# Performance work log

Hardware: AMD Instinct MI355X
Metric: run time of the kernel (lower is better)

## Reference

```python
import jax, jax.numpy as jnp
import numpy as np

N_HEAD = 16
MASK_VALUE = -10000.0


def setup_inputs() -> dict:
    key = jax.random.key(0)
    k1, k2, k3 = jax.random.split(key, 3)
    B, S, D = 2, 2048, 1024
    x = jax.random.normal(k1, (B, S, D), dtype=jnp.float32)
    W_qkv = jax.random.normal(k2, (D, 3 * D), dtype=jnp.float32) * 0.02
    b_qkv = jnp.zeros((3 * D,), dtype=jnp.float32)
    W_out = jax.random.normal(k3, (D, D), dtype=jnp.float32) * 0.02
    b_out = jnp.zeros((D,), dtype=jnp.float32)
    return {"x": x, "W_qkv": W_qkv, "b_qkv": b_qkv, "W_out": W_out, "b_out": b_out}


def reference(x, W_qkv, b_qkv, W_out, b_out):
    B, S, D = x.shape
    H = N_HEAD
    hd = D // H
    # fused QKV projection
    qkv = x @ W_qkv + b_qkv                      # [B, S, 3D]
    q, k, v = jnp.split(qkv, 3, axis=-1)
    # split heads -> [B, H, S, hd]
    def split_heads(t):
        return t.reshape(B, S, H, hd).transpose(0, 2, 1, 3)
    q, k, v = split_heads(q), split_heads(k), split_heads(v)
    # scaled causal attention with explicit mask-fill (matches ops.attention)
    scale = 1.0 / jnp.sqrt(jnp.asarray(hd, dtype=x.dtype))
    w = jnp.einsum('bhqd,bhkd->bhqk', q, k) * scale   # [B, H, S, S]
    causal = jnp.tril(jnp.ones((S, S), dtype=bool))    # [S, S]
    w = jnp.where(causal, w, jnp.asarray(MASK_VALUE, dtype=w.dtype))
    a = jax.nn.softmax(w, axis=-1)
    o = jnp.einsum('bhqk,bhkd->bhqd', a, v)            # [B, H, S, hd]
    # merge heads -> [B, S, D]
    o = o.transpose(0, 2, 1, 3).reshape(B, S, D)
    out = o @ W_out + b_out
    return out
```

## Files before the change

kernel.cpp:

```cpp
#include <hip/hip_runtime.h>
#include <hip/hip_bf16.h>
#include <stdint.h>

#define BATCH 2
#define SEQ   2048
#define DIM   1024
#define NH    16
#define HD    64
#define MVAL  (-10000.0f)

#if __has_builtin(__builtin_amdgcn_exp2f)
#define EXP2(x) __builtin_amdgcn_exp2f(x)
#define QSCALE  (0.125f * 1.44269504f)
#else
#define EXP2(x) __expf(x)
#define QSCALE  0.125f
#endif

typedef __attribute__((ext_vector_type(8))) short bf16x8;
typedef __attribute__((ext_vector_type(4))) float f32x4;
typedef unsigned short u16;

static __device__ __forceinline__ u16 f2bf(float f) {
  union { float f; uint32_t u; } c; c.f = f;
  uint32_t x = c.u;
  return (u16)((x + 0x7fffu + ((x >> 16) & 1u)) >> 16);
}

static __device__ __forceinline__ uint32_t pk2(float a, float b) {
  __hip_bfloat162 h = __float22bfloat162_rn(make_float2(a, b));
  union { __hip_bfloat162 h; uint32_t u; } c; c.h = h;
  return c.u;
}

static __device__ __forceinline__ int swz128(int row, int chunk) {
  return row * 128 + (((chunk ^ (row & 7)) & 7) << 4);
}

static __device__ __forceinline__ void gload_lds16(const void* g, void* l) {
  __builtin_amdgcn_global_load_lds((const __attribute__((address_space(1))) void*)g,
                                   (__attribute__((address_space(3))) void*)l, 16, 0, 0);
}

__global__ void cvt_kernel(const float* __restrict__ in, u16* __restrict__ out, int n4) {
  int i = blockIdx.x * blockDim.x + threadIdx.x;
  if (i < n4) {
    float4 v = reinterpret_cast<const float4*>(in)[i];
    reinterpret_cast<uint2*>(out)[i] = make_uint2(pk2(v.x, v.y), pk2(v.z, v.w));
  }
}

__global__ void transpose_cvt_kernel(const float* __restrict__ in, u16* __restrict__ out,
                                     int R, int C) {
  __shared__ float tile[32][33];
  int c0 = blockIdx.x * 32, r0 = blockIdx.y * 32;
  int tx = threadIdx.x, ty = threadIdx.y;
#pragma unroll
  for (int i = 0; i < 32; i += 8)
    tile[ty + i][tx] = in[(size_t)(r0 + ty + i) * C + c0 + tx];
  __syncthreads();
#pragma unroll
  for (int i = 0; i < 32; i += 8)
    out[(size_t)(c0 + ty + i) * R + r0 + tx] = f2bf(tile[tx][ty + i]);
}

__global__ void vtrans_kernel(const u16* __restrict__ Vi, u16* __restrict__ Vo) {
  __shared__ __align__(16) char t[8192];
  int tid = threadIdx.x;
  int bh = blockIdx.y, s0 = blockIdx.x * 64;
  const u16* src = Vi + ((size_t)bh * SEQ + s0) * HD;
#pragma unroll
  for (int i = 0; i < 2; i++) {
    int r = i * 32 + (tid >> 3), ch = tid & 7;
    uint4 v = *reinterpret_cast<const uint4*>(src + (size_t)r * HD + ch * 8);
    *reinterpret_cast<uint4*>(t + swz128(r, ch)) = v;
  }
  __syncthreads();
  int d = tid >> 2, sc = tid & 3;
  u16 vals[16];
#pragma unroll
  for (int j = 0; j < 16; j++) {
    int s = sc * 16 + j;
    vals[j] = *reinterpret_cast<const u16*>(
        t + s * 128 + ((((d >> 3) ^ (s & 7)) & 7) << 4) + (d & 7) * 2);
  }
  u16* dst = Vo + ((size_t)bh * HD + d) * SEQ + s0 + sc * 16;
  *reinterpret_cast<uint4*>(dst) = *reinterpret_cast<const uint4*>(vals);
  *reinterpret_cast<uint4*>(dst + 8) = *reinterpret_cast<const uint4*>(vals + 8);
}

template <int EPI>
__global__ __launch_bounds__(256, 2) void gemm_bt_kernel(
    const u16* __restrict__ A, const u16* __restrict__ Bt,
    const float* __restrict__ bias, float* __restrict__ Cout,
    u16* __restrict__ Qo, u16* __restrict__ Ko, u16* __restrict__ Vo,
    int M, int N, int K) {
  __shared__ __align__(16) char lds[32768];
  char* As = lds;
  char* Bs = lds + 16384;
  int tid = threadIdx.x;
  int lane = tid & 63, l15 = lane & 15, l4 = lane >> 4;
  int w = tid >> 6, wr = w >> 1, wc = w & 1;
  int m0 = blockIdx.y * 128, n0 = blockIdx.x * 128;
  int srow = tid >> 3, sch = tid & 7;
  int sc_swz = ((sch ^ (srow & 7)) << 3);

  const u16* Ap = A + (size_t)(m0 + srow) * K + sc_swz;
  const u16* Bp = Bt + (size_t)(n0 + srow) * K + sc_swz;

  f32x4 acc[4][4] = {};

  for (int k0 = 0; k0 < K; k0 += 64) {
    __syncthreads();
#pragma unroll
    for (int i = 0; i < 4; i++) {
      gload_lds16(Ap + (size_t)i * 32 * K + k0, As + i * 4096 + tid * 16);
      gload_lds16(Bp + (size_t)i * 32 * K + k0, Bs + i * 4096 + tid * 16);
    }
    __syncthreads();
#pragma unroll
    for (int ks = 0; ks < 2; ks++) {
      int ch = ks * 4 + l4;
      bf16x8 af[4], bfv[4];
#pragma unroll
      for (int mi = 0; mi < 4; mi++)
        af[mi] = *reinterpret_cast<const bf16x8*>(As + swz128(wr * 64 + mi * 16 + l15, ch));
#pragma unroll
      for (int nj = 0; nj < 4; nj++)
        bfv[nj] = *reinterpret_cast<const bf16x8*>(Bs + swz128(wc * 64 + nj * 16 + l15, ch));
#pragma unroll
      for (int nj = 0; nj < 4; nj++)
#pragma unroll
        for (int mi = 0; mi < 4; mi++)
          acc[nj][mi] = __builtin_amdgcn_mfma_f32_16x16x32_bf16(bfv[nj], af[mi], acc[nj][mi], 0, 0, 0);
    }
  }

#pragma unroll
  for (int nj = 0; nj < 4; nj++) {
    int nb = n0 + wc * 64 + nj * 16 + l4 * 4;
    float4 bv = *reinterpret_cast<const float4*>(bias + nb);
#pragma unroll
    for (int mi = 0; mi < 4; mi++) {
      int m = m0 + wr * 64 + mi * 16 + l15;
      f32x4 a = acc[nj][mi];
      float v0 = a[0] + bv.x, v1 = a[1] + bv.y, v2 = a[2] + bv.z, v3 = a[3] + bv.w;
      if (EPI == 1) {
        *reinterpret_cast<float4*>(Cout + (size_t)m * N + nb) = make_float4(v0, v1, v2, v3);
      } else {
        int b = m >> 11, s = m & 2047;
        int sec = nb >> 10, c = nb & 1023, h = c >> 6, d = c & 63;
        size_t bh = (size_t)(b * NH + h);
        u16* dst;
        float scl;
        if (sec == 0)      { dst = Qo; scl = QSCALE; }
        else if (sec == 1) { dst = Ko; scl = 1.0f; }
        else               { dst = Vo; scl = 1.0f; }
        *reinterpret_cast<uint2*>(dst + (bh * SEQ + s) * HD + d) =
            make_uint2(pk2(v0 * scl, v1 * scl), pk2(v2 * scl, v3 * scl));
      }
    }
  }
}

__global__ __launch_bounds__(256, 2) void attn_kernel(
    const u16* __restrict__ Q, const u16* __restrict__ K,
    const u16* __restrict__ Vt, u16* __restrict__ O) {
  __shared__ __align__(16) char lds[81920];
  int tid = threadIdx.x, lane = tid & 63, w = tid >> 6;
  int l15 = lane & 15, l4 = lane >> 4;
  int sub = w & 1, par = w >> 1;
  int blk = blockIdx.x;
  int bh = (blk & 7) * 4 + ((blk >> 3) & 3);
  int p = blk >> 5;
  const u16* Qh = Q + (size_t)bh * SEQ * HD;
  const u16* Kh = K + (size_t)bh * SEQ * HD;
  const u16* Vh = Vt + (size_t)bh * HD * SEQ;
  char* Pw = lds + 65536 + w * 4096;
  int srow = tid >> 3, sch = tid & 7;
  int b_ = bh >> 4, h_ = bh & 15;

  bf16x8 onesf;
#pragma unroll
  for (int j = 0; j < 8; j++) onesf[j] = (short)0x3F80;

  auto stageKV = [&](int b, int T) {
    const u16* Kt = Kh + (size_t)T * 128 * HD;
    const u16* Vs = Vh + (size_t)T * 128;
    char* Kb = lds + b * 16384;
    char* Vb = lds + 32768 + b * 16384;
#pragma unroll
    for (int i = 0; i < 4; i++) {
      int row = i * 32 + srow;
      int c = (sch ^ (row & 7)) << 3;
      gload_lds16(Kt + (size_t)row * HD + c, Kb + row * 128 + sch * 16);
    }
#pragma unroll
    for (int sv = 0; sv < 2; sv++)
#pragma unroll
      for (int i = 0; i < 2; i++) {
        int d = i * 32 + srow;
        int c = (sch ^ (d & 7)) << 3;
        gload_lds16(Vs + (size_t)d * SEQ + sv * 64 + c, Vb + sv * 8192 + d * 128 + sch * 16);
      }
  };

  int buf = 0;
  stageKV(0, 0);
  __syncthreads();

  for (int pass = 0; pass < 2; pass++) {
    int qt = (pass == 0) ? (31 - p) : p;
    int nT = (qt + 2) >> 1;
    int qb = qt * 64 + sub * 32;

    bf16x8 qf[2][2];
#pragma unroll
    for (int mi = 0; mi < 2; mi++)
#pragma unroll
      for (int ks = 0; ks < 2; ks++)
        qf[mi][ks] = *reinterpret_cast<const bf16x8*>(
            Qh + (size_t)(qb + mi * 16 + l15) * HD + ks * 32 + l4 * 8);

    float mrun[2] = {-1e30f, -1e30f};
    f32x4 oacc[4][2] = {};
    f32x4 acc_l[2] = {};

    for (int T = 0; T < nT; T++) {
      int nxt = (T + 1 < nT) ? (T + 1) : (pass == 0 ? 0 : -1);
      if (nxt >= 0) stageKV(buf ^ 1, nxt);

      char* Kw = lds + buf * 16384 + par * 8192;
      char* Vw = lds + 32768 + buf * 16384 + par * 8192;
      int kvb = T * 128 + par * 64;

      f32x4 s[4][2] = {};
      __builtin_amdgcn_s_setprio(1);
#pragma unroll
      for (int ks = 0; ks < 2; ks++)
#pragma unroll
        for (int nj = 0; nj < 4; nj++) {
          bf16x8 kf = *reinterpret_cast<const bf16x8*>(Kw + swz128(nj * 16 + l15, ks * 4 + l4));
#pragma unroll
          for (int mi = 0; mi < 2; mi++)
            s[nj][mi] = __builtin_amdgcn_mfma_f32_16x16x32_bf16(kf, qf[mi][ks], s[nj][mi], 0, 0, 0);
        }
      __builtin_amdgcn_s_setprio(0);

      bf16x8 vf[4][2];
#pragma unroll
      for (int ks = 0; ks < 2; ks++)
#pragma unroll
        for (int nd = 0; nd < 4; nd++)
          vf[nd][ks] = *reinterpret_cast<const bf16x8*>(Vw + swz128(nd * 16 + l15, ks * 4 + l4));

      if (kvb + 63 > qb) {
#pragma unroll
        for (int nj = 0; nj < 4; nj++)
#pragma unroll
          for (int mi = 0; mi < 2; mi++) {
            int qg = qb + mi * 16 + l15;
#pragma unroll
            for (int r = 0; r < 4; r++) {
              int kg = kvb + nj * 16 + l4 * 4 + r;
              if (kg > qg) s[nj][mi][r] = MVAL;
            }
          }
      }

      float mt[2];
#pragma unroll
      for (int mi = 0; mi < 2; mi++) {
        float m = s[0][mi][0];
#pragma unroll
        for (int nj = 0; nj < 4; nj++)
#pragma unroll
          for (int r = 0; r < 4; r++) m = fmaxf(m, s[nj][mi][r]);
        m = fmaxf(m, __shfl_xor(m, 16));
        m = fmaxf(m, __shfl_xor(m, 32));
        mt[mi] = m;
      }

      if (!__all((mt[0] <= mrun[0]) & (mt[1] <= mrun[1]))) {
#pragma unroll
        for (int mi = 0; mi < 2; mi++) {
          float mnew = fmaxf(mrun[mi], mt[mi]);
          float alpha = EXP2(mrun[mi] - mnew);
          mrun[mi] = mnew;
#pragma unroll
          for (int nd = 0; nd < 4; nd++)
#pragma unroll
            for (int r = 0; r < 4; r++) oacc[nd][mi][r] *= alpha;
#pragma unroll
          for (int r = 0; r < 4; r++) acc_l[mi][r] *= alpha;
        }
      }

#pragma unroll
      for (int mi = 0; mi < 2; mi++) {
        int prow = mi * 16 + l15;
#pragma unroll
        for (int nj = 0; nj < 4; nj++) {
          float p0 = EXP2(s[nj][mi][0] - mrun[mi]);
          float p1 = EXP2(s[nj][mi][1] - mrun[mi]);
          float p2 = EXP2(s[nj][mi][2] - mrun[mi]);
          float p3 = EXP2(s[nj][mi][3] - mrun[mi]);
          int chunk = nj * 2 + (l4 >> 1);
          char* dst = Pw + prow * 128 + (((chunk ^ (prow & 7)) & 7) << 4) + (l4 & 1) * 8;
          *reinterpret_cast<uint2*>(dst) = make_uint2(pk2(p0, p1), pk2(p2, p3));
        }
      }

      asm volatile("s_waitcnt lgkmcnt(0)" ::: "memory");
      __builtin_amdgcn_sched_barrier(0);

      bf16x8 pf[2][2];
#pragma unroll
      for (int mi = 0; mi < 2; mi++)
#pragma unroll
        for (int ks = 0; ks < 2; ks++)
          pf[mi][ks] = *reinterpret_cast<const bf16x8*>(Pw + swz128(mi * 16 + l15, ks * 4 + l4));

      __builtin_amdgcn_s_setprio(1);
#pragma unroll
      for (int ks = 0; ks < 2; ks++) {
#pragma unroll
        for (int nd = 0; nd < 4; nd++)
#pragma unroll
          for (int mi = 0; mi < 2; mi++)
            oacc[nd][mi] = __builtin_amdgcn_mfma_f32_16x16x32_bf16(vf[nd][ks], pf[mi][ks], oacc[nd][mi], 0, 0, 0);
#pragma unroll
        for (int mi = 0; mi < 2; mi++)
          acc_l[mi] = __builtin_amdgcn_mfma_f32_16x16x32_bf16(onesf, pf[mi][ks], acc_l[mi], 0, 0, 0);
      }
      __builtin_amdgcn_s_setprio(0);

      __syncthreads();
      buf ^= 1;
    }

    char* Xo = lds + (buf ^ 1) * 16384;
    float* Xml = (float*)(lds + 65536);
    if (par == 1) {
#pragma unroll
      for (int mi = 0; mi < 2; mi++) {
        int row = sub * 32 + mi * 16 + l15;
        if (l4 == 0) {
          Xml[row * 2] = mrun[mi];
          Xml[row * 2 + 1] = acc_l[mi][0];
        }
#pragma unroll
        for (int nd = 0; nd < 4; nd++)
          *reinterpret_cast<f32x4*>(Xo + row * 256 + (((nd * 4 + l4) ^ (row & 7)) << 4)) =
              oacc[nd][mi];
      }
    }
    __syncthreads();
    if (par == 0) {
#pragma unroll
      for (int mi = 0; mi < 2; mi++) {
        int row = sub * 32 + mi * 16 + l15;
        float mB = Xml[row * 2], lB = Xml[row * 2 + 1];
        float m = fmaxf(mrun[mi], mB);
        float wA = EXP2(mrun[mi] - m), wB = EXP2(mB - m);
        float linv = 1.0f / (acc_l[mi][0] * wA + lB * wB);
        float fA = wA * linv, fB = wB * linv;
        u16* orow = O + ((size_t)b_ * SEQ + qt * 64 + sub * 32 + mi * 16 + l15) * DIM + h_ * HD;
#pragma unroll
        for (int nd = 0; nd < 4; nd++) {
          f32x4 ob = *reinterpret_cast<const f32x4*>(
              Xo + row * 256 + (((nd * 4 + l4) ^ (row & 7)) << 4));
          float o0 = oacc[nd][mi][0] * fA + ob[0] * fB;
          float o1 = oacc[nd][mi][1] * fA + ob[1] * fB;
          float o2 = oacc[nd][mi][2] * fA + ob[2] * fB;
          float o3 = oacc[nd][mi][3] * fA + ob[3] * fB;
          *reinterpret_cast<uint2*>(orow + nd * 16 + l4 * 4) = make_uint2(pk2(o0, o1), pk2(o2, o3));
        }
      }
    }
    __syncthreads();
  }
}

extern "C" void kernel_launch(void* const* d_in, const int* in_sizes, int n_in,
                              void* d_out, int out_size, void* d_ws, size_t ws_size,
                              hipStream_t stream) {
  const float* x     = (const float*)d_in[0];
  const float* W_qkv = (const float*)d_in[1];
  const float* b_qkv = (const float*)d_in[2];
  const float* W_out = (const float*)d_in[3];
  const float* b_out = (const float*)d_in[4];
  float* out = (float*)d_out;
  char* ws = (char*)d_ws;

  u16* xb    = (u16*)(ws);
  u16* WqkvT = (u16*)(ws + 8388608);
  u16* WoutT = (u16*)(ws + 8388608 + 6291456);
  u16* Qb    = (u16*)(ws + 16777216);
  u16* Kb    = (u16*)(ws + 16777216 + 8388608);
  u16* Vtb   = (u16*)(ws + 16777216 + 2 * 8388608);
  u16* Ob    = (u16*)(ws + 16777216 + 3 * 8388608);
  u16* Vraw  = Ob;

  cvt_kernel<<<4096, 256, 0, stream>>>(x, xb, BATCH * SEQ * DIM / 4);
  transpose_cvt_kernel<<<dim3(3 * DIM / 32, DIM / 32), dim3(32, 8), 0, stream>>>(
      W_qkv, WqkvT, DIM, 3 * DIM);
  transpose_cvt_kernel<<<dim3(DIM / 32, DIM / 32), dim3(32, 8), 0, stream>>>(
      W_out, WoutT, DIM, DIM);
  gemm_bt_kernel<0><<<dim3(3 * DIM / 128, BATCH * SEQ / 128), 256, 0, stream>>>(
      xb, WqkvT, b_qkv, nullptr, Qb, Kb, Vraw, BATCH * SEQ, 3 * DIM, DIM);
  vtrans_kernel<<<dim3(SEQ / 64, BATCH * NH), 256, 0, stream>>>(Vraw, Vtb);
  attn_kernel<<<512, 256, 0, stream>>>(Qb, Kb, Vtb, Ob);
  gemm_bt_kernel<1><<<dim3(DIM / 128, BATCH * SEQ / 128), 256, 0, stream>>>(
      Ob, WoutT, b_out, out, nullptr, nullptr, nullptr, BATCH * SEQ, DIM, DIM);
}
```

Baseline: 124.1 us.

## Load K/V fragments directly from global memory and drop LDS double-buffering in attention

The attention kernel no longer stages K and V tiles into shared memory with async loads and a double buffer. Each wave now reads its K and V MFMA fragments straight from global memory. Work is reorganised so each block runs two independent 32-row query jobs, with the two wave parities splitting the KV tiles and merging through a smaller LDS scratch area. This cuts LDS use and per-tile block barriers, allowing three blocks per CU, but it gives up shared K/V reuse across waves and the overlap from prefetching, so global and L2 traffic rises.

New measurement: 150.0 us. +20.9%, slower.

```diff
diff --git a/kernel.cpp b/kernel.cpp
--- a/kernel.cpp
+++ b/kernel.cpp
@@ -163,56 +163,33 @@
   }
 }
 
-__global__ __launch_bounds__(256, 2) void attn_kernel(
+__global__ __launch_bounds__(256, 3) void attn_kernel(
     const u16* __restrict__ Q, const u16* __restrict__ K,
     const u16* __restrict__ Vt, u16* __restrict__ O) {
-  __shared__ __align__(16) char lds[81920];
+  __shared__ __align__(16) char lds[33280];
   int tid = threadIdx.x, lane = tid & 63, w = tid >> 6;
   int l15 = lane & 15, l4 = lane >> 4;
-  int sub = w & 1, par = w >> 1;
+  int par = w & 1, jobIdx = w >> 1;
   int blk = blockIdx.x;
-  int bh = (blk & 7) * 4 + ((blk >> 3) & 3);
-  int p = blk >> 5;
+  int r = blk >> 3;
+  int bh = (blk & 7) * 4 + (r & 3);
+  int p = (r >> 2) + 16 * jobIdx;
   const u16* Qh = Q + (size_t)bh * SEQ * HD;
   const u16* Kh = K + (size_t)bh * SEQ * HD;
   const u16* Vh = Vt + (size_t)bh * HD * SEQ;
-  char* Pw = lds + 65536 + w * 4096;
-  int srow = tid >> 3, sch = tid & 7;
+  char* Pw = lds + w * 4096;
+  char* Xo = lds + 16384 + jobIdx * 8448;
+  float* Xml = (float*)(Xo + 8192);
   int b_ = bh >> 4, h_ = bh & 15;
 
   bf16x8 onesf;
 #pragma unroll
   for (int j = 0; j < 8; j++) onesf[j] = (short)0x3F80;
 
-  auto stageKV = [&](int b, int T) {
-    const u16* Kt = Kh + (size_t)T * 128 * HD;
-    const u16* Vs = Vh + (size_t)T * 128;
-    char* Kb = lds + b * 16384;
-    char* Vb = lds + 32768 + b * 16384;
-#pragma unroll
-    for (int i = 0; i < 4; i++) {
-      int row = i * 32 + srow;
-      int c = (sch ^ (row & 7)) << 3;
-      gload_lds16(Kt + (size_t)row * HD + c, Kb + row * 128 + sch * 16);
-    }
-#pragma unroll
-    for (int sv = 0; sv < 2; sv++)
-#pragma unroll
-      for (int i = 0; i < 2; i++) {
-        int d = i * 32 + srow;
-        int c = (sch ^ (d & 7)) << 3;
-        gload_lds16(Vs + (size_t)d * SEQ + sv * 64 + c, Vb + sv * 8192 + d * 128 + sch * 16);
-      }
-  };
-
-  int buf = 0;
-  stageKV(0, 0);
-  __syncthreads();
-
   for (int pass = 0; pass < 2; pass++) {
-    int qt = (pass == 0) ? (31 - p) : p;
-    int nT = (qt + 2) >> 1;
-    int qb = qt * 64 + sub * 32;
+    int c = (pass == 0) ? (63 - p) : p;
+    int nkt = (c + 2) >> 1;
+    int qb = c * 32;
 
     bf16x8 qf[2][2];
 #pragma unroll
@@ -226,33 +203,36 @@
     f32x4 oacc[4][2] = {};
     f32x4 acc_l[2] = {};
 
-    for (int T = 0; T < nT; T++) {
-      int nxt = (T + 1 < nT) ? (T + 1) : (pass == 0 ? 0 : -1);
-      if (nxt >= 0) stageKV(buf ^ 1, nxt);
-
-      char* Kw = lds + buf * 16384 + par * 8192;
-      char* Vw = lds + 32768 + buf * 16384 + par * 8192;
-      int kvb = T * 128 + par * 64;
+    for (int T = par; T < nkt; T += 2) {
+      int kvb = T * 64;
+      const u16* Kt = Kh + (size_t)kvb * HD;
+
+      bf16x8 kf[4][2];
+#pragma unroll
+      for (int nj = 0; nj < 4; nj++)
+#pragma unroll
+        for (int ks = 0; ks < 2; ks++)
+          kf[nj][ks] = *reinterpret_cast<const bf16x8*>(
+              Kt + (size_t)(nj * 16 + l15) * HD + ks * 32 + l4 * 8);
 
       f32x4 s[4][2] = {};
       __builtin_amdgcn_s_setprio(1);
 #pragma unroll
       for (int ks = 0; ks < 2; ks++)
 #pragma unroll
-        for (int nj = 0; nj < 4; nj++) {
-          bf16x8 kf = *reinterpret_cast<const bf16x8*>(Kw + swz128(nj * 16 + l15, ks * 4 + l4));
+        for (int nj = 0; nj < 4; nj++)
 #pragma unroll
           for (int mi = 0; mi < 2; mi++)
-            s[nj][mi] = __builtin_amdgcn_mfma_f32_16x16x32_bf16(kf, qf[mi][ks], s[nj][mi], 0, 0, 0);
-        }
+            s[nj][mi] = __builtin_amdgcn_mfma_f32_16x16x32_bf16(kf[nj][ks], qf[mi][ks], s[nj][mi], 0, 0, 0);
       __builtin_amdgcn_s_setprio(0);
 
       bf16x8 vf[4][2];
 #pragma unroll
-      for (int ks = 0; ks < 2; ks++)
-#pragma unroll
-        for (int nd = 0; nd < 4; nd++)
-          vf[nd][ks] = *reinterpret_cast<const bf16x8*>(Vw + swz128(nd * 16 + l15, ks * 4 + l4));
+      for (int nd = 0; nd < 4; nd++)
+#pragma unroll
+        for (int ks = 0; ks < 2; ks++)
+          vf[nd][ks] = *reinterpret_cast<const bf16x8*>(
+              Vh + (size_t)(nd * 16 + l15) * SEQ + kvb + ks * 32 + l4 * 8);
 
       if (kvb + 63 > qb) {
 #pragma unroll
@@ -261,9 +241,9 @@
           for (int mi = 0; mi < 2; mi++) {
             int qg = qb + mi * 16 + l15;
 #pragma unroll
-            for (int r = 0; r < 4; r++) {
-              int kg = kvb + nj * 16 + l4 * 4 + r;
-              if (kg > qg) s[nj][mi][r] = MVAL;
+            for (int rr = 0; rr < 4; rr++) {
+              int kg = kvb + nj * 16 + l4 * 4 + rr;
+              if (kg > qg) s[nj][mi][rr] = MVAL;
             }
           }
       }
@@ -275,7 +255,7 @@
 #pragma unroll
         for (int nj = 0; nj < 4; nj++)
 #pragma unroll
-          for (int r = 0; r < 4; r++) m = fmaxf(m, s[nj][mi][r]);
+          for (int rr = 0; rr < 4; rr++) m = fmaxf(m, s[nj][mi][rr]);
         m = fmaxf(m, __shfl_xor(m, 16));
         m = fmaxf(m, __shfl_xor(m, 32));
         mt[mi] = m;
@@ -290,9 +270,9 @@
 #pragma unroll
           for (int nd = 0; nd < 4; nd++)
 #pragma unroll
-            for (int r = 0; r < 4; r++) oacc[nd][mi][r] *= alpha;
-#pragma unroll
-          for (int r = 0; r < 4; r++) acc_l[mi][r] *= alpha;
+            for (int rr = 0; rr < 4; rr++) oacc[nd][mi][rr] *= alpha;
+#pragma unroll
+          for (int rr = 0; rr < 4; rr++) acc_l[mi][rr] *= alpha;
         }
       }
 
@@ -334,17 +314,13 @@
           acc_l[mi] = __builtin_amdgcn_mfma_f32_16x16x32_bf16(onesf, pf[mi][ks], acc_l[mi], 0, 0, 0);
       }
       __builtin_amdgcn_s_setprio(0);
-
-      __syncthreads();
-      buf ^= 1;
-    }
-
-    char* Xo = lds + (buf ^ 1) * 16384;
-    float* Xml = (float*)(lds + 65536);
+    }
+
+    __syncthreads();
     if (par == 1) {
 #pragma unroll
       for (int mi = 0; mi < 2; mi++) {
-        int row = sub * 32 + mi * 16 + l15;
+        int row = mi * 16 + l15;
         if (l4 == 0) {
           Xml[row * 2] = mrun[mi];
           Xml[row * 2 + 1] = acc_l[mi][0];
@@ -359,13 +335,13 @@
     if (par == 0) {
 #pragma unroll
       for (int mi = 0; mi < 2; mi++) {
-        int row = sub * 32 + mi * 16 + l15;
+        int row = mi * 16 + l15;
         float mB = Xml[row * 2], lB = Xml[row * 2 + 1];
         float m = fmaxf(mrun[mi], mB);
         float wA = EXP2(mrun[mi] - m), wB = EXP2(mB - m);
         float linv = 1.0f / (acc_l[mi][0] * wA + lB * wB);
         float fA = wA * linv, fB = wB * linv;
-        u16* orow = O + ((size_t)b_ * SEQ + qt * 64 + sub * 32 + mi * 16 + l15) * DIM + h_ * HD;
+        u16* orow = O + ((size_t)b_ * SEQ + qb + mi * 16 + l15) * DIM + h_ * HD;
 #pragma unroll
         for (int nd = 0; nd < 4; nd++) {
           f32x4 ob = *reinterpret_cast<const f32x4*>(
@@ -378,7 +354,6 @@
         }
       }
     }
-    __syncthreads();
   }
 }
 
```
